# Kernel optimization log

Hardware: AMD Instinct MI355X
Metric: run time of the kernel (lower is better)

The kernel has to match this reference:

```python
import jax, jax.numpy as jnp
import numpy as np
import math

B, S, D, H = 4, 2048, 1024, 16
HD = D // H  # 64
FF = 4096
EPS = 1e-5


def layer_norm(x, g, b):
    mu = jnp.mean(x, axis=-1, keepdims=True)
    var = jnp.mean(jnp.square(x - mu), axis=-1, keepdims=True)
    return (x - mu) * jax.lax.rsqrt(var + EPS) * g + b


def setup_inputs() -> dict:
    key = jax.random.key(0)
    ks = jax.random.split(key, 16)
    sc = 0.02
    return {
        "x": jax.random.normal(ks[0], (B, S, D), dtype=jnp.float32),
        "Wq": jax.random.normal(ks[1], (H, D, HD), dtype=jnp.float32) * sc,
        "bq": jnp.zeros((H, HD), dtype=jnp.float32),
        "Wk": jax.random.normal(ks[2], (H, D, HD), dtype=jnp.float32) * sc,
        "bk": jnp.zeros((H, HD), dtype=jnp.float32),
        "Wv": jax.random.normal(ks[3], (H, D, HD), dtype=jnp.float32) * sc,
        "bv": jnp.zeros((H, HD), dtype=jnp.float32),
        "Wo": jax.random.normal(ks[4], (D, D), dtype=jnp.float32) * sc,
        "bo": jnp.zeros((D,), dtype=jnp.float32),
        "W1": jax.random.normal(ks[5], (D, FF), dtype=jnp.float32) * sc,
        "b1": jnp.zeros((FF,), dtype=jnp.float32),
        "W2": jax.random.normal(ks[6], (FF, D), dtype=jnp.float32) * sc,
        "b2": jnp.zeros((D,), dtype=jnp.float32),
        "ln1_g": jnp.ones((D,), dtype=jnp.float32),
        "ln1_b": jnp.zeros((D,), dtype=jnp.float32),
        "ln2_g": jnp.ones((D,), dtype=jnp.float32),
        "ln2_b": jnp.zeros((D,), dtype=jnp.float32),
    }


def reference(x, Wq, bq, Wk, bk, Wv, bv, Wo, bo, W1, b1, W2, b2, ln1_g, ln1_b, ln2_g, ln2_b):
    b, s, d = x.shape
    h1 = layer_norm(x, ln1_g, ln1_b)
    # per-head Q/K/V linears, vectorized over heads: [b,h,s,hd]
    q = jnp.einsum('bsd,hde->bhse', h1, Wq) + bq[None, :, None, :]
    k = jnp.einsum('bsd,hde->bhse', h1, Wk) + bk[None, :, None, :]
    v = jnp.einsum('bsd,hde->bhse', h1, Wv) + bv[None, :, None, :]
    scores = jnp.einsum('bhqe,bhke->bhqk', q, k) / math.sqrt(q.shape[-1])
    causal = jnp.tril(jnp.ones((s, s), dtype=bool))
    scores = jnp.where(causal[None, None], scores, -jnp.inf)
    weights = jax.nn.softmax(scores, axis=-1)
    attn = jnp.einsum('bhqk,bhke->bhqe', weights, v)
    # concat heads (head order = torch concat dim=-1)
    attn = attn.transpose(0, 2, 1, 3).reshape(b, s, d)
    x = x + attn @ Wo + bo
    h2 = layer_norm(x, ln2_g, ln2_b)
    y = jax.nn.gelu(h2 @ W1 + b1, approximate=False)
    y = jax.nn.gelu(y @ W2 + b2, approximate=False)
    return x + y
```

## Files before the change

### kernel.cpp

```cpp
#include <hip/hip_runtime.h>
#include <cstdint>
#include <cstddef>


#define DI __device__ __forceinline__

typedef __attribute__((ext_vector_type(8))) __bf16 bf16x8;
typedef __attribute__((ext_vector_type(4))) float floatx4;

static constexpr int Bn = 4, Sn = 2048, Dn = 1024, Hn = 16, HDn = 64, FFn = 4096;
static constexpr int NTOK = Bn * Sn;
static constexpr int D3 = 3 * Dn;

DI float bf2f(unsigned short u) { return __uint_as_float(((unsigned int)u) << 16); }
DI unsigned short f2bf(float f) {
  unsigned int u = __float_as_uint(f);
  u += 0x7FFFu + ((u >> 16) & 1u);
  return (unsigned short)(u >> 16);
}
DI float gelu_f(float v) { return 0.5f * v * (1.0f + erff(v * 0.70710678118654752f)); }
DI bf16x8 ld8(const unsigned short* p) { return *(const bf16x8*)p; }
DI floatx4 mfma16(bf16x8 a, bf16x8 b, floatx4 c) {
  return __builtin_amdgcn_mfma_f32_16x16x32_bf16(a, b, c, 0, 0, 0);
}
DI void g2l16(const unsigned short* g, unsigned short* l) {
  __builtin_amdgcn_global_load_lds((__attribute__((address_space(1))) void*)g,
                                   (__attribute__((address_space(3))) void*)l,
                                   16, 0, 0);
}
DI float ldin(const void* p, size_t idx, bool f32) {
  return f32 ? ((const float*)p)[idx] : bf2f(((const unsigned short*)p)[idx]);
}
DI int swz16(int row, int col) {
  return (row << 6) + ((((col >> 3) ^ row ^ (row >> 3)) & 7) << 3) + (col & 7);
}

__global__ void detect_kernel(const unsigned short* __restrict__ x,
                              int* __restrict__ flag) {
  int t = threadIdx.x;
  int cnt = 0;
  for (int i = t; i < 1024; i += 64) {
    unsigned short u = x[2 * i];
    int e = (u >> 7) & 0xFF;
    cnt += (e >= 96 && e <= 142) ? 1 : 0;
  }
  #pragma unroll
  for (int off = 32; off >= 1; off >>= 1) cnt += __shfl_xor(cnt, off);
  if (t == 0) *flag = (cnt < 820) ? 1 : 0;
}

__global__ void vec_prep(const void* bq, const void* bk, const void* bv,
                         const void* bo, const void* b1, const void* b2,
                         const void* g1, const void* be1, const void* g2,
                         const void* be2, unsigned short* __restrict__ dst,
                         const int* __restrict__ flag) {
  int i = blockIdx.x * 256 + threadIdx.x;
  if (i >= 13312) return;
  const bool f32 = *flag != 0;
  const void* src; int off;
  if      (i < 1024)  { src = bq;  off = i; }
  else if (i < 2048)  { src = bk;  off = i - 1024; }
  else if (i < 3072)  { src = bv;  off = i - 2048; }
  else if (i < 4096)  { src = bo;  off = i - 3072; }
  else if (i < 8192)  { src = b1;  off = i - 4096; }
  else if (i < 9216)  { src = b2;  off = i - 8192; }
  else if (i < 10240) { src = g1;  off = i - 9216; }
  else if (i < 11264) { src = be1; off = i - 10240; }
  else if (i < 12288) { src = g2;  off = i - 11264; }
  else                { src = be2; off = i - 12288; }
  dst[i] = f2bf(ldin(src, off, f32));
}

__global__ void transpose_kernel(const void* __restrict__ src,
                                 unsigned short* __restrict__ dst, int K, int N,
                                 const int* __restrict__ flag) {
  __shared__ unsigned short tile[64][65];
  const bool f32 = *flag != 0;
  int kb = blockIdx.y * 64, nb = blockIdx.x * 64;
  for (int i = threadIdx.x; i < 4096; i += 256) {
    int r = i >> 6, c = i & 63;
    tile[r][c] = f2bf(ldin(src, (size_t)(kb + r) * N + nb + c, f32));
  }
  __syncthreads();
  for (int i = threadIdx.x; i < 4096; i += 256) {
    int r = i >> 6, c = i & 63;
    dst[(size_t)(nb + r) * K + kb + c] = tile[c][r];
  }
}

__global__ void qkvT_kernel(const void* __restrict__ Wq,
                            const void* __restrict__ Wk,
                            const void* __restrict__ Wv,
                            unsigned short* __restrict__ WT,
                            const int* __restrict__ flag) {
  __shared__ unsigned short tile[64][65];
  const bool f32 = *flag != 0;
  const void* src = blockIdx.z == 0 ? Wq : (blockIdx.z == 1 ? Wk : Wv);
  int h = blockIdx.y, d0 = blockIdx.x * 64;
  size_t base = (size_t)h * (Dn * HDn);
  for (int i = threadIdx.x; i < 4096; i += 256) {
    int r = i >> 6, c = i & 63;
    tile[r][c] = f2bf(ldin(src, base + (size_t)(d0 + r) * 64 + c, f32));
  }
  __syncthreads();
  for (int i = threadIdx.x; i < 4096; i += 256) {
    int r = i >> 6, c = i & 63;
    WT[(size_t)(blockIdx.z * 1024 + h * 64 + r) * 1024 + d0 + c] = tile[c][r];
  }
}

__global__ __launch_bounds__(256) void ln_kernel(const void* __restrict__ x,
                                                 const unsigned short* __restrict__ g,
                                                 const unsigned short* __restrict__ b,
                                                 unsigned short* __restrict__ out,
                                                 const int* __restrict__ flag) {
  const bool f32 = flag ? (*flag != 0) : true;
  int row = blockIdx.x, t = threadIdx.x;
  float v[4];
  if (f32) {
    float4 f = *(const float4*)((const float*)x + (size_t)row * Dn + t * 4);
    v[0] = f.x; v[1] = f.y; v[2] = f.z; v[3] = f.w;
  } else {
    ushort4 u = *(const ushort4*)((const unsigned short*)x + (size_t)row * Dn + t * 4);
    v[0] = bf2f(u.x); v[1] = bf2f(u.y); v[2] = bf2f(u.z); v[3] = bf2f(u.w);
  }
  float s = v[0] + v[1] + v[2] + v[3];
  float s2 = v[0] * v[0] + v[1] * v[1] + v[2] * v[2] + v[3] * v[3];
  #pragma unroll
  for (int off = 32; off >= 1; off >>= 1) {
    s += __shfl_xor(s, off);
    s2 += __shfl_xor(s2, off);
  }
  __shared__ float red[8];
  int wv = t >> 6, ln = t & 63;
  if (ln == 0) { red[wv] = s; red[4 + wv] = s2; }
  __syncthreads();
  s = red[0] + red[1] + red[2] + red[3];
  s2 = red[4] + red[5] + red[6] + red[7];
  float mu = s * (1.0f / 1024.0f);
  float var = s2 * (1.0f / 1024.0f) - mu * mu;
  float rs = rsqrtf(fmaxf(var, 0.0f) + 1e-5f);
  ushort4 gg = *(const ushort4*)(g + t * 4);
  ushort4 bb = *(const ushort4*)(b + t * 4);
  ushort4 o;
  o.x = f2bf((v[0] - mu) * rs * bf2f(gg.x) + bf2f(bb.x));
  o.y = f2bf((v[1] - mu) * rs * bf2f(gg.y) + bf2f(bb.y));
  o.z = f2bf((v[2] - mu) * rs * bf2f(gg.z) + bf2f(bb.z));
  o.w = f2bf((v[3] - mu) * rs * bf2f(gg.w) + bf2f(bb.w));
  *(ushort4*)(out + (size_t)row * Dn + t * 4) = o;
}

enum { EPI_BIAS_BF16 = 0, EPI_WO = 1, EPI_GELU = 2, EPI_FF2 = 3 };

template <int EPI>
__global__ __launch_bounds__(256, 3) void gemm_kernel(
    const unsigned short* __restrict__ A, const unsigned short* __restrict__ BT,
    const unsigned short* __restrict__ bias, const void* __restrict__ residv,
    const float* __restrict__ resid_f, unsigned short* __restrict__ Cb,
    float* __restrict__ Cf, const int* __restrict__ flag, int M, int N, int K) {
  __shared__ unsigned short As[128 * 32];
  __shared__ unsigned short Bs[128 * 32];
  const int m0 = blockIdx.y * 128, n0 = blockIdx.x * 128;
  const int w = threadIdx.x >> 6, lane = threadIdx.x & 63;
  const int waveM = (w >> 1) * 64, waveN = (w & 1) * 64;
  const int m16 = lane & 15, quad = lane >> 4;
  const bool rf32 = flag && (*flag != 0);

  const int srow = w * 32 + (lane >> 2);
  const int scol = (lane & 3) * 8;
  const unsigned short* Ag = A + (size_t)(m0 + srow) * K + scol;
  const unsigned short* Bg = BT + (size_t)(n0 + srow) * K + scol;
  unsigned short* Al = As + srow * 32 + scol;
  unsigned short* Bl = Bs + srow * 32 + scol;
  const size_t rowstep = (size_t)16 * K;

  floatx4 acc[4][4];
  #pragma unroll
  for (int i = 0; i < 4; i++)
    #pragma unroll
    for (int j = 0; j < 4; j++) acc[i][j] = floatx4{0.f, 0.f, 0.f, 0.f};

  for (int k0 = 0; k0 < K; k0 += 32) {
    g2l16(Ag, Al);
    g2l16(Ag + rowstep, Al + 16 * 32);
    g2l16(Bg, Bl);
    g2l16(Bg + rowstep, Bl + 16 * 32);
    Ag += 32; Bg += 32;
    __syncthreads();
    bf16x8 af[4], bfv[4];
    #pragma unroll
    for (int mt = 0; mt < 4; mt++)
      af[mt] = ld8(As + (waveM + mt * 16 + m16) * 32 + quad * 8);
    #pragma unroll
    for (int nt = 0; nt < 4; nt++)
      bfv[nt] = ld8(Bs + (waveN + nt * 16 + m16) * 32 + quad * 8);
    #pragma unroll
    for (int mt = 0; mt < 4; mt++)
      #pragma unroll
      for (int nt = 0; nt < 4; nt++)
        acc[mt][nt] = mfma16(af[mt], bfv[nt], acc[mt][nt]);
    __syncthreads();
  }

  #pragma unroll
  for (int mt = 0; mt < 4; mt++) {
    #pragma unroll
    for (int nt = 0; nt < 4; nt++) {
      const int col = n0 + waveN + nt * 16 + m16;
      const float bcol = bf2f(bias[col]);
      #pragma unroll
      for (int r = 0; r < 4; r++) {
        const int row = m0 + waveM + mt * 16 + quad * 4 + r;
        const size_t idx = (size_t)row * N + col;
        float v = acc[mt][nt][r] + bcol;
        if constexpr (EPI == EPI_BIAS_BF16) {
          Cb[idx] = f2bf(v);
        } else if constexpr (EPI == EPI_WO) {
          float rv = rf32 ? ((const float*)residv)[idx]
                          : bf2f(((const unsigned short*)residv)[idx]);
          Cf[idx] = v + rv;
        } else if constexpr (EPI == EPI_GELU) {
          Cb[idx] = f2bf(gelu_f(v));
        } else {
          float ov = gelu_f(v) + resid_f[idx];
          if (rf32) Cf[idx] = ov;
          else      Cb[idx] = f2bf(ov);
        }
      }
    }
  }
}

__global__ __launch_bounds__(256, 4) void attn_kernel(
    const unsigned short* __restrict__ qkv, unsigned short* __restrict__ attn) {
  const int qt = (int)gridDim.x - 1 - (int)blockIdx.x;
  const int bh = blockIdx.y;
  const int b = bh >> 4, h = bh & 15;
  const int tid = threadIdx.x;
  const int w = tid >> 6, lane = tid & 63;
  const int m16 = lane & 15, quad = lane >> 4;

  __shared__ unsigned short Ks[2][4096];
  __shared__ unsigned short Vt[2][4096];
  __shared__ unsigned short Ps[4][1024];
  unsigned short* PsW = Ps[w];

  const int qrow = qt * 64 + w * 16 + m16;
  const unsigned short* qp = qkv + (size_t)(b * Sn + qrow) * D3 + h * 64 + quad * 8;
  const bf16x8 qf0 = ld8(qp), qf1 = ld8(qp + 32);

  floatx4 acc_o[4];
  #pragma unroll
  for (int nt = 0; nt < 4; nt++) acc_o[nt] = floatx4{0.f, 0.f, 0.f, 0.f};
  float lsum[4] = {0.f, 0.f, 0.f, 0.f};

  const int kr = tid >> 3, kc = (tid & 7) * 8;
  const int vk = (tid >> 3) * 2, ve = (tid & 7) * 8;

  uint4 kreg0, kreg1, vreg0, vreg1;
  const unsigned short* const kvroot = qkv + (size_t)(b * Sn) * D3 + h * 64;

  {
    const unsigned short* base = kvroot;
    kreg0 = *(const uint4*)(base + (size_t)kr * D3 + 1024 + kc);
    kreg1 = *(const uint4*)(base + (size_t)(kr + 32) * D3 + 1024 + kc);
    vreg0 = *(const uint4*)(base + (size_t)vk * D3 + 2048 + ve);
    vreg1 = *(const uint4*)(base + (size_t)(vk + 1) * D3 + 2048 + ve);
  }

  for (int kt = 0; kt <= qt; ++kt) {
    const int pb = kt & 1;
    *(uint4*)(Ks[pb] + swz16(kr, kc)) = kreg0;
    *(uint4*)(Ks[pb] + swz16(kr + 32, kc)) = kreg1;
    {
      const unsigned short* a0 = (const unsigned short*)&vreg0;
      const unsigned short* a1 = (const unsigned short*)&vreg1;
      #pragma unroll
      for (int i = 0; i < 8; i++) {
        unsigned int word = (unsigned int)a0[i] | ((unsigned int)a1[i] << 16);
        *(unsigned int*)(Vt[pb] + swz16(ve + i, vk)) = word;
      }
    }
    __syncthreads();
    if (kt < qt) {
      const unsigned short* base = kvroot + (size_t)(kt + 1) * 64 * D3;
      kreg0 = *(const uint4*)(base + (size_t)kr * D3 + 1024 + kc);
      kreg1 = *(const uint4*)(base + (size_t)(kr + 32) * D3 + 1024 + kc);
      vreg0 = *(const uint4*)(base + (size_t)vk * D3 + 2048 + ve);
      vreg1 = *(const uint4*)(base + (size_t)(vk + 1) * D3 + 2048 + ve);
    }

    floatx4 sa[4];
    #pragma unroll
    for (int nt = 0; nt < 4; nt++) {
      bf16x8 k0 = ld8(Ks[pb] + swz16(nt * 16 + m16, quad * 8));
      bf16x8 k1 = ld8(Ks[pb] + swz16(nt * 16 + m16, 32 + quad * 8));
      floatx4 t = mfma16(qf0, k0, floatx4{0.f, 0.f, 0.f, 0.f});
      sa[nt] = mfma16(qf1, k1, t);
    }

    #pragma unroll
    for (int r = 0; r < 4; r++) {
      const int qgr = qt * 64 + w * 16 + quad * 4 + r;
      #pragma unroll
      for (int nt = 0; nt < 4; nt++) {
        const int kgc = kt * 64 + nt * 16 + m16;
        float pv = (kgc <= qgr) ? __expf(sa[nt][r] * 0.125f) : 0.0f;
        lsum[r] += pv;
        PsW[swz16(quad * 4 + r, nt * 16 + m16)] = f2bf(pv);
      }
    }
    const bf16x8 p0 = ld8(PsW + swz16(m16, quad * 8));
    const bf16x8 p1 = ld8(PsW + swz16(m16, 32 + quad * 8));
    #pragma unroll
    for (int nt = 0; nt < 4; nt++) {
      bf16x8 v0 = ld8(Vt[pb] + swz16(nt * 16 + m16, quad * 8));
      bf16x8 v1 = ld8(Vt[pb] + swz16(nt * 16 + m16, 32 + quad * 8));
      acc_o[nt] = mfma16(p0, v0, acc_o[nt]);
      acc_o[nt] = mfma16(p1, v1, acc_o[nt]);
    }
  }

  #pragma unroll
  for (int r = 0; r < 4; r++) {
    #pragma unroll
    for (int off = 1; off < 16; off <<= 1) lsum[r] += __shfl_xor(lsum[r], off);
  }

  #pragma unroll
  for (int r = 0; r < 4; r++) {
    const float inv = 1.0f / fmaxf(lsum[r], 1e-20f);
    const size_t orow = (size_t)(b * Sn + qt * 64 + w * 16 + quad * 4 + r) * Dn + h * 64;
    #pragma unroll
    for (int nt = 0; nt < 4; nt++)
      attn[orow + nt * 16 + m16] = f2bf(acc_o[nt][r] * inv);
  }
}

extern "C" void kernel_launch(void* const* d_in, const int* in_sizes, int n_in,
                              void* d_out, int out_size, void* d_ws, size_t ws_size,
                              hipStream_t stream) {
  (void)in_sizes; (void)n_in; (void)out_size; (void)ws_size;
  const void* x    = d_in[0];
  const void* Wq   = d_in[1];
  const void* bq   = d_in[2];
  const void* Wk   = d_in[3];
  const void* bk   = d_in[4];
  const void* Wv   = d_in[5];
  const void* bv   = d_in[6];
  const void* Wo   = d_in[7];
  const void* bo   = d_in[8];
  const void* W1   = d_in[9];
  const void* b1   = d_in[10];
  const void* W2   = d_in[11];
  const void* b2   = d_in[12];
  const void* ln1g = d_in[13];
  const void* ln1b = d_in[14];
  const void* ln2g = d_in[15];
  const void* ln2b = d_in[16];
  char* ws = (char*)d_ws;

  constexpr size_t OFF_WTQKV = 0;
  constexpr size_t OFF_WOT   = OFF_WTQKV + (size_t)D3 * Dn * 2;
  constexpr size_t OFF_W1T   = OFF_WOT + (size_t)Dn * Dn * 2;
  constexpr size_t OFF_W2T   = OFF_W1T + (size_t)FFn * Dn * 2;
  constexpr size_t OFF_VEC   = OFF_W2T + (size_t)Dn * FFn * 2;
  constexpr size_t OFF_FLAG  = OFF_VEC + 32768;
  constexpr size_t OFF_H     = OFF_FLAG + 256;
  constexpr size_t OFF_QKV   = OFF_H + (size_t)NTOK * Dn * 2;
  constexpr size_t OFF_ATTN  = OFF_QKV + (size_t)NTOK * D3 * 2;
  constexpr size_t OFF_X2    = OFF_ATTN + (size_t)NTOK * Dn * 2;
  constexpr size_t OFF_Y1    = OFF_QKV;

  unsigned short* WTqkv = (unsigned short*)(ws + OFF_WTQKV);
  unsigned short* WoT   = (unsigned short*)(ws + OFF_WOT);
  unsigned short* W1T   = (unsigned short*)(ws + OFF_W1T);
  unsigned short* W2T   = (unsigned short*)(ws + OFF_W2T);
  unsigned short* vec   = (unsigned short*)(ws + OFF_VEC);
  int*            flag  = (int*)(ws + OFF_FLAG);
  unsigned short* hbuf  = (unsigned short*)(ws + OFF_H);
  unsigned short* qkvb  = (unsigned short*)(ws + OFF_QKV);
  unsigned short* attnb = (unsigned short*)(ws + OFF_ATTN);
  float*          x2    = (float*)(ws + OFF_X2);
  unsigned short* y1    = (unsigned short*)(ws + OFF_Y1);

  detect_kernel<<<1, 64, 0, stream>>>((const unsigned short*)x, flag);

  vec_prep<<<52, 256, 0, stream>>>(bq, bk, bv, bo, b1, b2, ln1g, ln1b, ln2g,
                                   ln2b, vec, flag);
  qkvT_kernel<<<dim3(16, 16, 3), 256, 0, stream>>>(Wq, Wk, Wv, WTqkv, flag);
  transpose_kernel<<<dim3(16, 16), 256, 0, stream>>>(Wo, WoT, 1024, 1024, flag);
  transpose_kernel<<<dim3(64, 16), 256, 0, stream>>>(W1, W1T, 1024, 4096, flag);
  transpose_kernel<<<dim3(16, 64), 256, 0, stream>>>(W2, W2T, 4096, 1024, flag);

  ln_kernel<<<NTOK, 256, 0, stream>>>(x, vec + 9216, vec + 10240, hbuf, flag);
  gemm_kernel<EPI_BIAS_BF16><<<dim3(D3 / 128, NTOK / 128), 256, 0, stream>>>(
      hbuf, WTqkv, vec + 0, nullptr, nullptr, qkvb, nullptr, nullptr,
      NTOK, D3, Dn);
  attn_kernel<<<dim3(Sn / 64, Bn * Hn), 256, 0, stream>>>(qkvb, attnb);
  gemm_kernel<EPI_WO><<<dim3(Dn / 128, NTOK / 128), 256, 0, stream>>>(
      attnb, WoT, vec + 3072, x, nullptr, nullptr, x2, flag, NTOK, Dn, Dn);
  ln_kernel<<<NTOK, 256, 0, stream>>>(x2, vec + 11264, vec + 12288, hbuf, nullptr);
  gemm_kernel<EPI_GELU><<<dim3(FFn / 128, NTOK / 128), 256, 0, stream>>>(
      hbuf, W1T, vec + 4096, nullptr, nullptr, y1, nullptr, nullptr,
      NTOK, FFn, Dn);
  gemm_kernel<EPI_FF2><<<dim3(Dn / 128, NTOK / 128), 256, 0, stream>>>(
      y1, W2T, vec + 8192, nullptr, x2, (unsigned short*)d_out, (float*)d_out,
      flag, NTOK, Dn, FFn);
}
```

Measured before the change: 655.2 us.

## Keep attention probabilities in registers via transposed QK^T and permuted K rows

The QK^T MFMA now takes its operands in swapped order, and K rows are written to shared memory in a permuted order. This makes the score fragment layout match the A-operand layout for the PV MFMA, so the per-wave shared-memory P buffer and its round trip through shared memory go away. Causal masking is applied only on the diagonal tile, exp uses exp2 with a folded scale, and bf16 packing uses a hardware pack instruction. Launch bounds rise to 5 blocks per CU to raise occupancy, which may put pressure on registers.

```diff
diff --git a/kernel.cpp b/kernel.cpp
--- a/kernel.cpp
+++ b/kernel.cpp
@@ -30,6 +30,11 @@
 }
 DI float ldin(const void* p, size_t idx, bool f32) {
   return f32 ? ((const float*)p)[idx] : bf2f(((const unsigned short*)p)[idx]);
+}
+DI unsigned int cvt_pk_bf16(float lo, float hi) {
+  unsigned int r;
+  asm("v_cvt_pk_bf16_f32 %0, %1, %2" : "=v"(r) : "v"(lo), "v"(hi));
+  return r;
 }
 DI int swz16(int row, int col) {
   return (row << 6) + ((((col >> 3) ^ row ^ (row >> 3)) & 7) << 3) + (col & 7);
@@ -231,7 +236,7 @@
   }
 }
 
-__global__ __launch_bounds__(256, 4) void attn_kernel(
+__global__ __launch_bounds__(256, 5) void attn_kernel(
     const unsigned short* __restrict__ qkv, unsigned short* __restrict__ attn) {
   const int qt = (int)gridDim.x - 1 - (int)blockIdx.x;
   const int bh = blockIdx.y;
@@ -242,19 +247,19 @@
 
   __shared__ unsigned short Ks[2][4096];
   __shared__ unsigned short Vt[2][4096];
-  __shared__ unsigned short Ps[4][1024];
-  unsigned short* PsW = Ps[w];
 
   const int qrow = qt * 64 + w * 16 + m16;
+  const int qloc = w * 16 + m16;
   const unsigned short* qp = qkv + (size_t)(b * Sn + qrow) * D3 + h * 64 + quad * 8;
   const bf16x8 qf0 = ld8(qp), qf1 = ld8(qp + 32);
 
   floatx4 acc_o[4];
   #pragma unroll
   for (int nt = 0; nt < 4; nt++) acc_o[nt] = floatx4{0.f, 0.f, 0.f, 0.f};
-  float lsum[4] = {0.f, 0.f, 0.f, 0.f};
+  float lsum = 0.f;
 
   const int kr = tid >> 3, kc = (tid & 7) * 8;
+  const int krs = (kr & 3) + (((kr >> 3) & 3) << 2) + (((kr >> 2) & 1) << 4);
   const int vk = (tid >> 3) * 2, ve = (tid & 7) * 8;
 
   uint4 kreg0, kreg1, vreg0, vreg1;
@@ -270,8 +275,8 @@
 
   for (int kt = 0; kt <= qt; ++kt) {
     const int pb = kt & 1;
-    *(uint4*)(Ks[pb] + swz16(kr, kc)) = kreg0;
-    *(uint4*)(Ks[pb] + swz16(kr + 32, kc)) = kreg1;
+    *(uint4*)(Ks[pb] + swz16(krs, kc)) = kreg0;
+    *(uint4*)(Ks[pb] + swz16(krs + 32, kc)) = kreg1;
     {
       const unsigned short* a0 = (const unsigned short*)&vreg0;
       const unsigned short* a1 = (const unsigned short*)&vreg1;
@@ -295,41 +300,50 @@
     for (int nt = 0; nt < 4; nt++) {
       bf16x8 k0 = ld8(Ks[pb] + swz16(nt * 16 + m16, quad * 8));
       bf16x8 k1 = ld8(Ks[pb] + swz16(nt * 16 + m16, 32 + quad * 8));
-      floatx4 t = mfma16(qf0, k0, floatx4{0.f, 0.f, 0.f, 0.f});
-      sa[nt] = mfma16(qf1, k1, t);
-    }
-
-    #pragma unroll
-    for (int r = 0; r < 4; r++) {
-      const int qgr = qt * 64 + w * 16 + quad * 4 + r;
+      floatx4 t = mfma16(k0, qf0, floatx4{0.f, 0.f, 0.f, 0.f});
+      sa[nt] = mfma16(k1, qf1, t);
+    }
+
+    if (kt == qt) {
       #pragma unroll
       for (int nt = 0; nt < 4; nt++) {
-        const int kgc = kt * 64 + nt * 16 + m16;
-        float pv = (kgc <= qgr) ? __expf(sa[nt][r] * 0.125f) : 0.0f;
-        lsum[r] += pv;
-        PsW[swz16(quad * 4 + r, nt * 16 + m16)] = f2bf(pv);
+        const int kb_ = (quad << 3) + ((nt & 1) << 2) + ((nt >> 1) << 5);
+        #pragma unroll
+        for (int r = 0; r < 4; r++)
+          if (kb_ + r > qloc) sa[nt][r] = -1e30f;
       }
     }
-    const bf16x8 p0 = ld8(PsW + swz16(m16, quad * 8));
-    const bf16x8 p1 = ld8(PsW + swz16(m16, 32 + quad * 8));
+
+    unsigned int pw[8];
+    #pragma unroll
+    for (int nt = 0; nt < 4; nt++) {
+      float e0 = __builtin_amdgcn_exp2f(sa[nt][0] * 0.18033688011112042f);
+      float e1 = __builtin_amdgcn_exp2f(sa[nt][1] * 0.18033688011112042f);
+      float e2 = __builtin_amdgcn_exp2f(sa[nt][2] * 0.18033688011112042f);
+      float e3 = __builtin_amdgcn_exp2f(sa[nt][3] * 0.18033688011112042f);
+      lsum += (e0 + e1) + (e2 + e3);
+      pw[2 * nt]     = cvt_pk_bf16(e0, e1);
+      pw[2 * nt + 1] = cvt_pk_bf16(e2, e3);
+    }
+    union { unsigned int u[4]; bf16x8 v; } pa0, pa1;
+    pa0.u[0] = pw[0]; pa0.u[1] = pw[1]; pa0.u[2] = pw[2]; pa0.u[3] = pw[3];
+    pa1.u[0] = pw[4]; pa1.u[1] = pw[5]; pa1.u[2] = pw[6]; pa1.u[3] = pw[7];
+
     #pragma unroll
     for (int nt = 0; nt < 4; nt++) {
       bf16x8 v0 = ld8(Vt[pb] + swz16(nt * 16 + m16, quad * 8));
       bf16x8 v1 = ld8(Vt[pb] + swz16(nt * 16 + m16, 32 + quad * 8));
-      acc_o[nt] = mfma16(p0, v0, acc_o[nt]);
-      acc_o[nt] = mfma16(p1, v1, acc_o[nt]);
-    }
-  }
+      acc_o[nt] = mfma16(pa0.v, v0, acc_o[nt]);
+      acc_o[nt] = mfma16(pa1.v, v1, acc_o[nt]);
+    }
+  }
+
+  lsum += __shfl_xor(lsum, 16);
+  lsum += __shfl_xor(lsum, 32);
 
   #pragma unroll
   for (int r = 0; r < 4; r++) {
-    #pragma unroll
-    for (int off = 1; off < 16; off <<= 1) lsum[r] += __shfl_xor(lsum[r], off);
-  }
-
-  #pragma unroll
-  for (int r = 0; r < 4; r++) {
-    const float inv = 1.0f / fmaxf(lsum[r], 1e-20f);
+    const float inv = 1.0f / fmaxf(__shfl(lsum, quad * 4 + r), 1e-20f);
     const size_t orow = (size_t)(b * Sn + qt * 64 + w * 16 + quad * 4 + r) * Dn + h * 64;
     #pragma unroll
     for (int nt = 0; nt < 4; nt++)
```

Result: slower. 852.3 us (+30.1%).
